# Optimization experiments

Measured on AMD Instinct MI355X. Metric: run time of the kernel, lower is better.

The kernel has to match this reference:

```python
import jax, jax.numpy as jnp
import numpy as np

B, C, L, NLAB, EMB, NFREQ, D = 256, 64, 512, 10, 256, 9, 8
FIN, FH, FOUT = 4 * C, C, C
P_TOTAL = FIN * FH + FH + FH * FOUT + FOUT + FIN * FOUT + FOUT


def _leaky(x):
    return jax.nn.leaky_relu(x, 0.2)


def _conv1d(x, w, b=None, pad=0):
    y = jax.lax.conv_general_dilated(x, w, (1,), [(pad, pad)], dimension_numbers=('NCH', 'OIH', 'NCH'))
    return y if b is None else y + b[None, :, None]


def _res1d(x, w0, b0, w1, b1, ws=None, pad=1):
    # GAN-stability style residual block: out = shortcut(x) + 0.1 * conv1(act(conv0(act(x))))
    xs = _conv1d(x, ws) if ws is not None else x
    dx = _conv1d(_leaky(x), w0, b0, pad)
    dx = _conv1d(_leaky(dx), w1, b1, pad)
    return xs + 0.1 * dx


def _pos_enc():
    # sinusoidal positional encoding, 2*NFREQ channels over L positions
    p = np.arange(L, dtype=np.float32)
    f = (np.pi / 2.0 ** np.arange(NFREQ, dtype=np.float32))[:, None]
    pe = np.concatenate([np.sin(f * p), np.cos(f * p)], axis=0)  # [2*NFREQ, L]
    return jnp.asarray(pe)


def _sobel_kernels():
    s = np.array([1.0, 2.0, 1.0], np.float32)
    d = np.array([-1.0, 0.0, 1.0], np.float32)
    kx = np.einsum('i,j,k->ijk', d, s, s)
    ky = np.einsum('i,j,k->ijk', s, d, s)
    kz = np.einsum('i,j,k->ijk', s, s, d)
    return jnp.asarray(np.stack([kx, ky, kz]))  # [3, 3, 3, 3]


def _sin_sobel(x, k):
    # depthwise 3D sobel along each axis, sin of gradients, concat with input -> 4C channels
    outs = [x]
    for i in range(3):
        w = jnp.broadcast_to(k[i][None, None], (C, 1, 3, 3, 3))
        g = jax.lax.conv_general_dilated(x, w, (1, 1, 1), [(1, 1)] * 3,
                                         dimension_numbers=('NCDHW', 'OIDHW', 'NCDHW'),
                                         feature_group_count=C)
        outs.append(jnp.sin(g))
    return jnp.concatenate(outs, axis=1)


def _inst_norm(x):
    m = x.mean(axis=(2, 3, 4), keepdims=True)
    v = x.var(axis=(2, 3, 4), keepdims=True)
    return (x - m) * jax.lax.rsqrt(v + 1e-5)


def _dyna(x, p):
    # hypernet-generated per-sample 1x1x1 residual conv block
    b = x.shape[0]
    xf = x.reshape(b, FIN, D * D * D)
    o = FIN * FH
    wh = p[:, :o].reshape(b, FH, FIN)
    bh = p[:, o:o + FH]; o += FH
    wl = p[:, o:o + FH * FOUT].reshape(b, FOUT, FH); o += FH * FOUT
    bl = p[:, o:o + FOUT]; o += FOUT
    ws = p[:, o:o + FIN * FOUT].reshape(b, FOUT, FIN); o += FIN * FOUT
    bs = p[:, o:o + FOUT]
    xs = jnp.einsum('boi,bis->bos', ws, xf) + bs[:, :, None]
    dx = _leaky(jnp.einsum('bhi,bis->bhs', wh, xf) + bh[:, :, None])
    dx = jnp.einsum('boh,bhs->bos', wl, dx) + bl[:, :, None]
    return (xs + 0.1 * dx).reshape(b, FOUT, D, D, D)


def _forward(codes, y, fc_w, fc_b, in_w0, in_b0, in_w1, in_b1, in_ws, leak, hyper_w, hyper_b,
             out_w0, out_b0, out_w1, out_b1, l1_w0, l1_b0, l1_w1, l1_b1,
             l2_w0, l2_b0, l2_w1, l2_b1, l2_ws):
    b = codes.shape[0]
    yemb = jax.nn.one_hot(y, NLAB, dtype=codes.dtype) @ fc_w.T + fc_b
    yemb = yemb / jnp.maximum(jnp.linalg.norm(yemb, axis=1, keepdims=True), 1e-12)
    pe = jnp.broadcast_to(_pos_enc()[None], (b, 2 * NFREQ, L))
    x = jnp.concatenate([codes, pe], axis=1)  # [B, C+2*NFREQ, L]
    x = _res1d(x, in_w0, in_b0, in_w1, in_b1, ws=in_ws)
    x = x.reshape(b, C, D, D, D)
    leak_c = jnp.clip(leak, 0.001, 1000.0)
    p = yemb @ hyper_w.T + hyper_b  # per-sample dynamic conv params [B, P_TOTAL]
    k = _sobel_kernels()
    for _ in range(8):
        xn = _inst_norm(x)
        xn = _sin_sobel(xn, k)
        xn = _dyna(xn, p)
        x = x + leak_c * xn
    x = x.reshape(b, C, L)
    x = _res1d(x, out_w0, out_b0, out_w1, out_b1)
    code_idx = jnp.argmax(codes, axis=1).reshape(b * L)
    logits = x.transpose(0, 2, 1).reshape(b * L, C)
    logp = jax.nn.log_softmax(logits, axis=-1)
    loss_cent = -jnp.take_along_axis(logp, code_idx[:, None], axis=1).mean()
    lat = _res1d(x, l1_w0, l1_b0, l1_w1, l1_b1, pad=0)
    lat = _res1d(lat, l2_w0, l2_b0, l2_w1, l2_b1, ws=l2_ws, pad=0)
    return lat[:, 0, :], loss_cent


def setup_inputs() -> dict:
    key = jax.random.key(0)
    ks = jax.random.split(key, 16)
    w = lambda k, s: 0.02 * jax.random.normal(k, s, jnp.float32)
    z = lambda s: jnp.zeros(s, jnp.float32)
    CIN = C + 2 * NFREQ  # 82
    return {
        'codes': jax.random.normal(ks[0], (B, C, L), jnp.float32),
        'y': jax.random.randint(ks[1], (B,), 0, NLAB),
        'fc_w': w(ks[2], (EMB, NLAB)), 'fc_b': z((EMB,)),
        'in_w0': w(ks[3], (C, CIN, 3)), 'in_b0': z((C,)),
        'in_w1': w(ks[4], (C, C, 3)), 'in_b1': z((C,)),
        'in_ws': w(ks[5], (C, CIN, 1)),
        'leak': jnp.asarray(0.1, jnp.float32),
        'hyper_w': w(ks[6], (P_TOTAL, EMB)), 'hyper_b': z((P_TOTAL,)),
        'out_w0': w(ks[7], (C, C, 3)), 'out_b0': z((C,)),
        'out_w1': w(ks[8], (C, C, 3)), 'out_b1': z((C,)),
        'l1_w0': w(ks[9], (C, C, 1)), 'l1_b0': z((C,)),
        'l1_w1': w(ks[10], (C, C, 1)), 'l1_b1': z((C,)),
        'l2_w0': w(ks[11], (1, C, 1)), 'l2_b0': z((1,)),
        'l2_w1': w(ks[12], (1, 1, 1)), 'l2_b1': z((1,)),
        'l2_ws': w(ks[13], (1, C, 1)),
    }


def reference(codes, y, fc_w, fc_b, in_w0, in_b0, in_w1, in_b1, in_ws, leak, hyper_w, hyper_b,
              out_w0, out_b0, out_w1, out_b1, l1_w0, l1_b0, l1_w1, l1_b1,
              l2_w0, l2_b0, l2_w1, l2_b1, l2_ws):
    return _forward(codes, y, fc_w, fc_b, in_w0, in_b0, in_w1, in_b1, in_ws, leak, hyper_w, hyper_b,
                    out_w0, out_b0, out_w1, out_b1, l1_w0, l1_b0, l1_w1, l1_b1,
                    l2_w0, l2_b0, l2_w1, l2_b1, l2_ws)
```

## Files before the change

### kernel.cpp

```cpp
#include <hip/hip_runtime.h>

#define B_ 256
#define C_ 64
#define L_ 512
#define CIN_ 82
#define NFREQ_ 9
#define EMB_ 256
#define NLAB_ 10
#define PT_ 37056
#define OFF_BH 16384
#define OFF_WL 16448
#define OFF_BL 20544
#define OFF_WS 20608
#define OFF_BS 36992
#define PI_F 3.14159265358979323846f

typedef short bh8 __attribute__((ext_vector_type(8)));
typedef float f32x4 __attribute__((ext_vector_type(4)));

__device__ inline float lrelu(float v){ return v > 0.f ? v : 0.2f*v; }

__device__ inline unsigned short f2bf(float f){
  unsigned u = __float_as_uint(f);
  u += 0x7FFFu + ((u >> 16) & 1u);
  return (unsigned short)(u >> 16);
}
__device__ inline float bf2f(unsigned short u){
  return __uint_as_float((unsigned)u << 16);
}
__device__ inline unsigned pk2(float a, float b){
  return (unsigned)f2bf(a) | ((unsigned)f2bf(b) << 16);
}
__device__ inline bh8 cvt8(float4 a, float4 b){
  bh8 r;
  r[0]=(short)f2bf(a.x); r[1]=(short)f2bf(a.y); r[2]=(short)f2bf(a.z); r[3]=(short)f2bf(a.w);
  r[4]=(short)f2bf(b.x); r[5]=(short)f2bf(b.y); r[6]=(short)f2bf(b.z); r[7]=(short)f2bf(b.w);
  return r;
}

__global__ __launch_bounds__(256) void k_yemb(const float* __restrict__ fc_w,
    const float* __restrict__ fc_b, const int* __restrict__ y,
    unsigned short* __restrict__ ybf, float* __restrict__ out){
  int b = blockIdx.x, e = threadIdx.x;
  int lab = y[b];
  float v = fc_w[e*NLAB_ + lab] + fc_b[e];
  __shared__ float red[256];
  red[e] = v*v; __syncthreads();
  for (int s = 128; s; s >>= 1){ if (e < s) red[e] += red[e+s]; __syncthreads(); }
  float nrm = fmaxf(sqrtf(red[0]), 1e-12f);
  ybf[(size_t)b*EMB_ + e] = f2bf(v / nrm);
  if (b == 0 && e == 0) out[B_*L_] = 0.f;
}

__global__ __launch_bounds__(256) void k_hyper(const float* __restrict__ hw,
    const float* __restrict__ hb, const unsigned short* __restrict__ ybf,
    unsigned short* __restrict__ p_bf){
  int tid = threadIdx.x;
  int wid = tid >> 6, lane = tid & 63, col = lane & 15, quad = lane >> 4;
  int j = blockIdx.x*64 + wid*16 + col;
  f32x4 acc[16];
  f32x4 z4 = {0.f,0.f,0.f,0.f};
  #pragma unroll
  for (int i = 0; i < 16; i++) acc[i] = z4;
  for (int k0 = 0; k0 < 256; k0 += 32){
    const float* hp = hw + (size_t)j*EMB_ + k0 + quad*8;
    bh8 bf = cvt8(*(const float4*)hp, *(const float4*)(hp+4));
    #pragma unroll
    for (int mt = 0; mt < 16; mt++){
      bh8 af = *(const bh8*)&ybf[(size_t)(mt*16 + col)*EMB_ + k0 + quad*8];
      acc[mt] = __builtin_amdgcn_mfma_f32_16x16x32_bf16(af, bf, acc[mt], 0, 0, 0);
    }
  }
  float hbv = hb[j];
  #pragma unroll
  for (int mt = 0; mt < 16; mt++){
    int b0 = mt*16 + quad*4;
    #pragma unroll
    for (int r = 0; r < 4; r++)
      p_bf[(size_t)(b0 + r)*PT_ + j] = f2bf(acc[mt][r] + hbv);
  }
}

__device__ inline float pe_raw(int fi, int l){
  if (fi < NFREQ_) return __sinf(PI_F / (float)(1 << fi) * (float)l);
  return __cosf(PI_F / (float)(1 << (fi - NFREQ_)) * (float)l);
}

__global__ __launch_bounds__(256) void k_conv_in1(const float* __restrict__ codes,
    const float* __restrict__ w0, const float* __restrict__ b0,
    unsigned short* __restrict__ t1bf){
  int b = blockIdx.x, l0 = blockIdx.y*128, tid = threadIdx.x;
  int wid = tid>>6, lane = tid&63, col = lane&15, quad = lane>>4;
  __shared__ __attribute__((aligned(16))) unsigned short xT[136][96];
  __shared__ __attribute__((aligned(16))) unsigned short wA[3][64][96];
  for (int i = tid; i < 64*96; i += 256){
    int m = i / 96, cin = i % 96;
    if (cin < CIN_){
      const float* s = w0 + (size_t)m*(CIN_*3) + cin*3;
      wA[0][m][cin] = f2bf(s[0]); wA[1][m][cin] = f2bf(s[1]); wA[2][m][cin] = f2bf(s[2]);
    } else { wA[0][m][cin] = 0; wA[1][m][cin] = 0; wA[2][m][cin] = 0; }
  }
  const float* cb = codes + (size_t)b*C_*L_;
  for (int i = tid; i < 96*34; i += 256){
    int c = i / 34, g = i % 34;
    int lg = l0 - 4 + 4*g;
    #pragma unroll
    for (int r2 = 0; r2 < 4; r2++){
      int l = lg + r2;
      float xv = 0.f;
      if (l >= 0 && l < L_){
        if (c < C_) xv = cb[(size_t)c*L_ + l];
        else if (c < CIN_) xv = pe_raw(c - C_, l);
      }
      xT[4*g + r2][c] = f2bf(lrelu(xv));
    }
  }
  __syncthreads();
  f32x4 z4 = {0.f,0.f,0.f,0.f};
  f32x4 acc[8];
  #pragma unroll
  for (int i = 0; i < 8; i++) acc[i] = z4;
  #pragma unroll
  for (int t = 0; t < 3; t++){
    #pragma unroll
    for (int k0 = 0; k0 < 96; k0 += 32){
      bh8 bfr[2];
      #pragma unroll
      for (int nt = 0; nt < 2; nt++)
        bfr[nt] = *(const bh8*)&xT[wid*32 + nt*16 + col + t + 3][k0 + quad*8];
      #pragma unroll
      for (int mt = 0; mt < 4; mt++){
        bh8 af = *(const bh8*)&wA[t][mt*16 + col][k0 + quad*8];
        #pragma unroll
        for (int nt = 0; nt < 2; nt++)
          acc[mt*2+nt] = __builtin_amdgcn_mfma_f32_16x16x32_bf16(af, bfr[nt], acc[mt*2+nt], 0,0,0);
      }
    }
  }
  #pragma unroll
  for (int mt = 0; mt < 4; mt++){
    int f0 = mt*16 + quad*4;
    float q0 = b0[f0], q1 = b0[f0+1], q2 = b0[f0+2], q3 = b0[f0+3];
    #pragma unroll
    for (int nt = 0; nt < 2; nt++){
      int l = l0 + wid*32 + nt*16 + col;
      f32x4 a = acc[mt*2+nt];
      uint2 o = { pk2(lrelu(a[0]+q0), lrelu(a[1]+q1)),
                  pk2(lrelu(a[2]+q2), lrelu(a[3]+q3)) };
      *(uint2*)&t1bf[((size_t)b*L_ + l)*64 + f0] = o;
    }
  }
}

__global__ __launch_bounds__(256) void k_conv_in2(const float* __restrict__ codes,
    const float* __restrict__ wsp, const float* __restrict__ w1, const float* __restrict__ b1,
    const unsigned short* __restrict__ t1bf, float* __restrict__ x){
  int b = blockIdx.x, l0 = blockIdx.y*128, tid = threadIdx.x;
  int wid = tid>>6, lane = tid&63, col = lane&15, quad = lane>>4;
  __shared__ __attribute__((aligned(16))) unsigned short xT[128][96];
  __shared__ __attribute__((aligned(16))) unsigned short wsA[64][96];
  __shared__ __attribute__((aligned(16))) unsigned short w1A[3][64][72];
  for (int i = tid; i < 64*96; i += 256){
    int m = i / 96, cin = i % 96;
    wsA[m][cin] = (cin < CIN_) ? f2bf(wsp[(size_t)m*CIN_ + cin]) : (unsigned short)0;
  }
  for (int i = tid; i < 64*64; i += 256){
    int m = i >> 6, cin = i & 63;
    const float* s = w1 + (size_t)m*192 + cin*3;
    w1A[0][m][cin] = f2bf(s[0]); w1A[1][m][cin] = f2bf(s[1]); w1A[2][m][cin] = f2bf(s[2]);
  }
  const float* cb = codes + (size_t)b*C_*L_;
  for (int i = tid; i < 96*32; i += 256){
    int c = i / 32, g = i % 32;
    int lg = l0 + 4*g;
    #pragma unroll
    for (int r2 = 0; r2 < 4; r2++){
      int l = lg + r2;
      float xv;
      if (c < C_) xv = cb[(size_t)c*L_ + l];
      else if (c < CIN_) xv = pe_raw(c - C_, l);
      else xv = 0.f;
      xT[4*g + r2][c] = f2bf(xv);
    }
  }
  __syncthreads();
  f32x4 z4 = {0.f,0.f,0.f,0.f};
  f32x4 accS[8], accD[8];
  #pragma unroll
  for (int i = 0; i < 8; i++){ accS[i] = z4; accD[i] = z4; }
  #pragma unroll
  for (int k0 = 0; k0 < 96; k0 += 32){
    bh8 bfr[2];
    #pragma unroll
    for (int nt = 0; nt < 2; nt++)
      bfr[nt] = *(const bh8*)&xT[wid*32 + nt*16 + col][k0 + quad*8];
    #pragma unroll
    for (int mt = 0; mt < 4; mt++){
      bh8 af = *(const bh8*)&wsA[mt*16 + col][k0 + quad*8];
      #pragma unroll
      for (int nt = 0; nt < 2; nt++)
        accS[mt*2+nt] = __builtin_amdgcn_mfma_f32_16x16x32_bf16(af, bfr[nt], accS[mt*2+nt], 0,0,0);
    }
  }
  bh8 zz8 = {0,0,0,0,0,0,0,0};
  #pragma unroll
  for (int t = 0; t < 3; t++){
    #pragma unroll
    for (int k0 = 0; k0 < 64; k0 += 32){
      bh8 bfr[2];
      #pragma unroll
      for (int nt = 0; nt < 2; nt++){
        int l = l0 + wid*32 + nt*16 + col + t - 1;
        bfr[nt] = (l >= 0 && l < L_)
          ? *(const bh8*)&t1bf[((size_t)b*L_ + l)*64 + k0 + quad*8] : zz8;
      }
      #pragma unroll
      for (int mt = 0; mt < 4; mt++){
        bh8 af = *(const bh8*)&w1A[t][mt*16 + col][k0 + quad*8];
        #pragma unroll
        for (int nt = 0; nt < 2; nt++)
          accD[mt*2+nt] = __builtin_amdgcn_mfma_f32_16x16x32_bf16(af, bfr[nt], accD[mt*2+nt], 0,0,0);
      }
    }
  }
  #pragma unroll
  for (int mt = 0; mt < 4; mt++){
    int f0 = mt*16 + quad*4;
    float q0 = b1[f0], q1 = b1[f0+1], q2 = b1[f0+2], q3 = b1[f0+3];
    #pragma unroll
    for (int nt = 0; nt < 2; nt++){
      int l = l0 + wid*32 + nt*16 + col;
      f32x4 s = accS[mt*2+nt], d = accD[mt*2+nt];
      size_t base = ((size_t)b*C_ + f0)*L_ + l;
      x[base]        = s[0] + 0.1f*(d[0] + q0);
      x[base + L_]   = s[1] + 0.1f*(d[1] + q1);
      x[base + 2*L_] = s[2] + 0.1f*(d[2] + q2);
      x[base + 3*L_] = s[3] + 0.1f*(d[3] + q3);
    }
  }
}

__global__ __launch_bounds__(256) void k_feat(const float* __restrict__ x,
    unsigned short* __restrict__ feat){
  int wid = threadIdx.x >> 6, lane = threadIdx.x & 63;
  int gi = blockIdx.x*4 + wid;
  const float* xr = x + (size_t)gi*L_ + lane*8;
  float4 v0 = *(const float4*)xr;
  float4 v1 = *(const float4*)(xr + 4);
  float r[8] = { v0.x, v0.y, v0.z, v0.w, v1.x, v1.y, v1.z, v1.w };
  float s1 = 0.f, s2 = 0.f;
  #pragma unroll
  for (int i = 0; i < 8; i++){ s1 += r[i]; s2 += r[i]*r[i]; }
  for (int m = 32; m; m >>= 1){ s1 += __shfl_xor(s1, m); s2 += __shfl_xor(s2, m); }
  float mean = s1 * (1.f/512.f);
  float rstd = rsqrtf(s2*(1.f/512.f) - mean*mean + 1e-5f);
  float xn[8];
  #pragma unroll
  for (int i = 0; i < 8; i++) xn[i] = (r[i] - mean) * rstd;

  size_t fb = ((size_t)(gi >> 6)*4*C_ + (gi & 63))*L_ + lane*8;
  { uint4 o = { pk2(xn[0],xn[1]), pk2(xn[2],xn[3]), pk2(xn[4],xn[5]), pk2(xn[6],xn[7]) };
    *(uint4*)(feat + fb) = o; }

  __shared__ float S[4][5][64][8];
  float A[8], Bv[8];
  A[0] = 2.f*xn[0] + xn[1];           Bv[0] = xn[1];
  #pragma unroll
  for (int i = 1; i < 7; i++){ A[i] = xn[i-1] + 2.f*xn[i] + xn[i+1]; Bv[i] = xn[i+1] - xn[i-1]; }
  A[7] = xn[6] + 2.f*xn[7];           Bv[7] = -xn[6];
  { float4 a0 = {A[0],A[1],A[2],A[3]}, a1 = {A[4],A[5],A[6],A[7]};
    float4 b0 = {Bv[0],Bv[1],Bv[2],Bv[3]}, b1 = {Bv[4],Bv[5],Bv[6],Bv[7]};
    *(float4*)&S[wid][0][lane][0] = a0; *(float4*)&S[wid][0][lane][4] = a1;
    *(float4*)&S[wid][1][lane][0] = b0; *(float4*)&S[wid][1][lane][4] = b1; }
  __syncthreads();

  int yy = lane & 7, zz = lane >> 3;
  int lm = (yy > 0) ? lane-1 : lane;  float wm = (yy > 0) ? 1.f : 0.f;
  int lp = (yy < 7) ? lane+1 : lane;  float wp = (yy < 7) ? 1.f : 0.f;
  float Am[8], Ap[8], Bm[8], Bp[8];
  { float4 u0, u1;
    u0 = *(const float4*)&S[wid][0][lm][0]; u1 = *(const float4*)&S[wid][0][lm][4];
    Am[0]=u0.x*wm; Am[1]=u0.y*wm; Am[2]=u0.z*wm; Am[3]=u0.w*wm; Am[4]=u1.x*wm; Am[5]=u1.y*wm; Am[6]=u1.z*wm; Am[7]=u1.w*wm;
    u0 = *(const float4*)&S[wid][0][lp][0]; u1 = *(const float4*)&S[wid][0][lp][4];
    Ap[0]=u0.x*wp; Ap[1]=u0.y*wp; Ap[2]=u0.z*wp; Ap[3]=u0.w*wp; Ap[4]=u1.x*wp; Ap[5]=u1.y*wp; Ap[6]=u1.z*wp; Ap[7]=u1.w*wp;
    u0 = *(const float4*)&S[wid][1][lm][0]; u1 = *(const float4*)&S[wid][1][lm][4];
    Bm[0]=u0.x*wm; Bm[1]=u0.y*wm; Bm[2]=u0.z*wm; Bm[3]=u0.w*wm; Bm[4]=u1.x*wm; Bm[5]=u1.y*wm; Bm[6]=u1.z*wm; Bm[7]=u1.w*wm;
    u0 = *(const float4*)&S[wid][1][lp][0]; u1 = *(const float4*)&S[wid][1][lp][4];
    Bp[0]=u0.x*wp; Bp[1]=u0.y*wp; Bp[2]=u0.z*wp; Bp[3]=u0.w*wp; Bp[4]=u1.x*wp; Bp[5]=u1.y*wp; Bp[6]=u1.z*wp; Bp[7]=u1.w*wp;
  }
  float Cv[8], Dv[8], Ev[8];
  #pragma unroll
  for (int i = 0; i < 8; i++){
    Cv[i] = Am[i] + 2.f*A[i] + Ap[i];
    Dv[i] = Ap[i] - Am[i];
    Ev[i] = Bm[i] + 2.f*Bv[i] + Bp[i];
  }
  { float4 c0={Cv[0],Cv[1],Cv[2],Cv[3]}, c1={Cv[4],Cv[5],Cv[6],Cv[7]};
    float4 d0={Dv[0],Dv[1],Dv[2],Dv[3]}, d1={Dv[4],Dv[5],Dv[6],Dv[7]};
    float4 e0={Ev[0],Ev[1],Ev[2],Ev[3]}, e1={Ev[4],Ev[5],Ev[6],Ev[7]};
    *(float4*)&S[wid][2][lane][0]=c0; *(float4*)&S[wid][2][lane][4]=c1;
    *(float4*)&S[wid][3][lane][0]=d0; *(float4*)&S[wid][3][lane][4]=d1;
    *(float4*)&S[wid][4][lane][0]=e0; *(float4*)&S[wid][4][lane][4]=e1; }
  __syncthreads();

  int zm = (zz > 0) ? lane-8 : lane;  float qm = (zz > 0) ? 1.f : 0.f;
  int zp = (zz < 7) ? lane+8 : lane;  float qp = (zz < 7) ? 1.f : 0.f;
  float g0[8], g1[8], g2[8];
  { float4 u0, u1, w0, w1;
    u0 = *(const float4*)&S[wid][2][zm][0]; u1 = *(const float4*)&S[wid][2][zm][4];
    w0 = *(const float4*)&S[wid][2][zp][0]; w1 = *(const float4*)&S[wid][2][zp][4];
    g0[0]=w0.x*qp-u0.x*qm; g0[1]=w0.y*qp-u0.y*qm; g0[2]=w0.z*qp-u0.z*qm; g0[3]=w0.w*qp-u0.w*qm;
    g0[4]=w1.x*qp-u1.x*qm; g0[5]=w1.y*qp-u1.y*qm; g0[6]=w1.z*qp-u1.z*qm; g0[7]=w1.w*qp-u1.w*qm;
    u0 = *(const float4*)&S[wid][3][zm][0]; u1 = *(const float4*)&S[wid][3][zm][4];
    w0 = *(const float4*)&S[wid][3][zp][0]; w1 = *(const float4*)&S[wid][3][zp][4];
    g1[0]=u0.x*qm+2.f*Dv[0]+w0.x*qp; g1[1]=u0.y*qm+2.f*Dv[1]+w0.y*qp;
    g1[2]=u0.z*qm+2.f*Dv[2]+w0.z*qp; g1[3]=u0.w*qm+2.f*Dv[3]+w0.w*qp;
    g1[4]=u1.x*qm+2.f*Dv[4]+w1.x*qp; g1[5]=u1.y*qm+2.f*Dv[5]+w1.y*qp;
    g1[6]=u1.z*qm+2.f*Dv[6]+w1.z*qp; g1[7]=u1.w*qm+2.f*Dv[7]+w1.w*qp;
    u0 = *(const float4*)&S[wid][4][zm][0]; u1 = *(const float4*)&S[wid][4][zm][4];
    w0 = *(const float4*)&S[wid][4][zp][0]; w1 = *(const float4*)&S[wid][4][zp][4];
    g2[0]=u0.x*qm+2.f*Ev[0]+w0.x*qp; g2[1]=u0.y*qm+2.f*Ev[1]+w0.y*qp;
    g2[2]=u0.z*qm+2.f*Ev[2]+w0.z*qp; g2[3]=u0.w*qm+2.f*Ev[3]+w0.w*qp;
    g2[4]=u1.x*qm+2.f*Ev[4]+w1.x*qp; g2[5]=u1.y*qm+2.f*Ev[5]+w1.y*qp;
    g2[6]=u1.z*qm+2.f*Ev[6]+w1.z*qp; g2[7]=u1.w*qm+2.f*Ev[7]+w1.w*qp;
  }
  { uint4 o = { pk2(__sinf(g0[0]),__sinf(g0[1])), pk2(__sinf(g0[2]),__sinf(g0[3])),
                pk2(__sinf(g0[4]),__sinf(g0[5])), pk2(__sinf(g0[6]),__sinf(g0[7])) };
    *(uint4*)(feat + fb + (size_t)C_*L_) = o; }
  { uint4 o = { pk2(__sinf(g1[0]),__sinf(g1[1])), pk2(__sinf(g1[2]),__sinf(g1[3])),
                pk2(__sinf(g1[4]),__sinf(g1[5])), pk2(__sinf(g1[6]),__sinf(g1[7])) };
    *(uint4*)(feat + fb + (size_t)2*C_*L_) = o; }
  { uint4 o = { pk2(__sinf(g2[0]),__sinf(g2[1])), pk2(__sinf(g2[2]),__sinf(g2[3])),
                pk2(__sinf(g2[4]),__sinf(g2[5])), pk2(__sinf(g2[6]),__sinf(g2[7])) };
    *(uint4*)(feat + fb + (size_t)3*C_*L_) = o; }
}

__global__ __launch_bounds__(256) void k_dyna(float* __restrict__ x,
    const unsigned short* __restrict__ feat, const unsigned short* __restrict__ p_bf,
    const float* __restrict__ leak){
  int b = blockIdx.x, tid = threadIdx.x;
  int wid = tid >> 6, lane = tid & 63, col = lane & 15, quad = lane >> 4;
  int s0 = blockIdx.y * 256;
  int ncol = s0 + wid*64;
  const unsigned short* pb = p_bf + (size_t)b*PT_;
  const unsigned short* fbase = feat + (size_t)b*4*C_*L_;
  __shared__ __attribute__((aligned(16))) unsigned short h_t[256][72];

  f32x4 zz4 = {0.f, 0.f, 0.f, 0.f};
  f32x4 acc_h[16], acc_s[16];
  #pragma unroll
  for (int i = 0; i < 16; i++){ acc_h[i] = zz4; acc_s[i] = zz4; }

  for (int k0 = 0; k0 < 256; k0 += 32){
    bh8 bf[4];
    #pragma unroll
    for (int nt = 0; nt < 4; nt++){
      const unsigned short* src = fbase + (size_t)(k0 + quad*8)*L_ + ncol + nt*16 + col;
      bh8 t;
      #pragma unroll
      for (int j = 0; j < 8; j++) t[j] = (short)src[(size_t)j*L_];
      bf[nt] = t;
    }
    #pragma unroll
    for (int mt = 0; mt < 4; mt++){
      int m = mt*16 + col;
      bh8 ah = *(const bh8*)&pb[(size_t)m*256 + k0 + quad*8];
      bh8 aw = *(const bh8*)&pb[OFF_WS + (size_t)m*256 + k0 + quad*8];
      #pragma unroll
      for (int nt = 0; nt < 4; nt++){
        acc_h[mt*4+nt] = __builtin_amdgcn_mfma_f32_16x16x32_bf16(ah, bf[nt], acc_h[mt*4+nt], 0, 0, 0);
        acc_s[mt*4+nt] = __builtin_amdgcn_mfma_f32_16x16x32_bf16(aw, bf[nt], acc_s[mt*4+nt], 0, 0, 0);
      }
    }
  }
  #pragma unroll
  for (int mt = 0; mt < 4; mt++){
    int f0 = mt*16 + quad*4;
    float bh0 = bf2f(pb[OFF_BH+f0]), bh1 = bf2f(pb[OFF_BH+f0+1]);
    float bh2 = bf2f(pb[OFF_BH+f0+2]), bh3 = bf2f(pb[OFF_BH+f0+3]);
    #pragma unroll
    for (int nt = 0; nt < 4; nt++){
      int n = wid*64 + nt*16 + col;
      f32x4 a = acc_h[mt*4+nt];
      uint2 o = { pk2(lrelu(a[0]+bh0), lrelu(a[1]+bh1)),
                  pk2(lrelu(a[2]+bh2), lrelu(a[3]+bh3)) };
      *(uint2*)&h_t[n][f0] = o;
    }
  }
  __syncthreads();
  f32x4 acc2[16];
  #pragma unroll
  for (int i = 0; i < 16; i++) acc2[i] = zz4;
  #pragma unroll
  for (int k0 = 0; k0 < 64; k0 += 32){
    bh8 hb[4];
    #pragma unroll
    for (int nt = 0; nt < 4; nt++){
      int n = wid*64 + nt*16 + col;
      hb[nt] = *(const bh8*)&h_t[n][k0 + quad*8];
    }
    #pragma unroll
    for (int mt = 0; mt < 4; mt++){
      bh8 al = *(const bh8*)&pb[OFF_WL + (size_t)(mt*16 + col)*64 + k0 + quad*8];
      #pragma unroll
      for (int nt = 0; nt < 4; nt++)
        acc2[mt*4+nt] = __builtin_amdgcn_mfma_f32_16x16x32_bf16(al, hb[nt], acc2[mt*4+nt], 0, 0, 0);
    }
  }
  float lk = fminf(fmaxf(leak[0], 0.001f), 1000.f);
  #pragma unroll
  for (int mt = 0; mt < 4; mt++){
    int f0 = mt*16 + quad*4;
    float bs0 = bf2f(pb[OFF_BS+f0]), bs1 = bf2f(pb[OFF_BS+f0+1]);
    float bs2 = bf2f(pb[OFF_BS+f0+2]), bs3 = bf2f(pb[OFF_BS+f0+3]);
    float bl0 = bf2f(pb[OFF_BL+f0]), bl1 = bf2f(pb[OFF_BL+f0+1]);
    float bl2 = bf2f(pb[OFF_BL+f0+2]), bl3 = bf2f(pb[OFF_BL+f0+3]);
    #pragma unroll
    for (int nt = 0; nt < 4; nt++){
      int s = ncol + nt*16 + col;
      f32x4 xs = acc_s[mt*4+nt], dx = acc2[mt*4+nt];
      float ov0 = xs[0] + bs0 + 0.1f*(dx[0] + bl0);
      float ov1 = xs[1] + bs1 + 0.1f*(dx[1] + bl1);
      float ov2 = xs[2] + bs2 + 0.1f*(dx[2] + bl2);
      float ov3 = xs[3] + bs3 + 0.1f*(dx[3] + bl3);
      size_t xi = ((size_t)b*C_ + f0)*L_ + s;
      x[xi]          += lk*ov0;
      x[xi + L_]     += lk*ov1;
      x[xi + 2*L_]   += lk*ov2;
      x[xi + 3*L_]   += lk*ov3;
    }
  }
}

__global__ __launch_bounds__(256) void k_conv_out1(const float* __restrict__ x,
    const float* __restrict__ w, const float* __restrict__ bias,
    unsigned short* __restrict__ t1bf){
  int b = blockIdx.x, l0 = blockIdx.y*128, tid = threadIdx.x;
  int wid = tid>>6, lane = tid&63, col = lane&15, quad = lane>>4;
  __shared__ __attribute__((aligned(16))) unsigned short xT[136][72];
  __shared__ __attribute__((aligned(16))) unsigned short wA[3][64][72];
  for (int i = tid; i < 64*64; i += 256){
    int m = i >> 6, cin = i & 63;
    const float* s = w + (size_t)m*192 + cin*3;
    wA[0][m][cin] = f2bf(s[0]); wA[1][m][cin] = f2bf(s[1]); wA[2][m][cin] = f2bf(s[2]);
  }
  const float* xb = x + (size_t)b*C_*L_;
  for (int i = tid; i < 64*34; i += 256){
    int c = i / 34, g = i % 34;
    int lg = l0 - 4 + 4*g;
    if (lg >= 0 && lg + 3 < L_){
      float4 f = *(const float4*)&xb[(size_t)c*L_ + lg];
      xT[4*g  ][c] = f2bf(lrelu(f.x));
      xT[4*g+1][c] = f2bf(lrelu(f.y));
      xT[4*g+2][c] = f2bf(lrelu(f.z));
      xT[4*g+3][c] = f2bf(lrelu(f.w));
    } else {
      #pragma unroll
      for (int r2 = 0; r2 < 4; r2++){
        int l = lg + r2;
        float v = (l >= 0 && l < L_) ? xb[(size_t)c*L_ + l] : 0.f;
        xT[4*g + r2][c] = f2bf(lrelu(v));
      }
    }
  }
  __syncthreads();
  f32x4 z4 = {0.f,0.f,0.f,0.f};
  f32x4 acc[8];
  #pragma unroll
  for (int i = 0; i < 8; i++) acc[i] = z4;
  #pragma unroll
  for (int t = 0; t < 3; t++){
    #pragma unroll
    for (int k0 = 0; k0 < 64; k0 += 32){
      bh8 bfr[2];
      #pragma unroll
      for (int nt = 0; nt < 2; nt++)
        bfr[nt] = *(const bh8*)&xT[wid*32 + nt*16 + col + t + 3][k0 + quad*8];
      #pragma unroll
      for (int mt = 0; mt < 4; mt++){
        bh8 af = *(const bh8*)&wA[t][mt*16 + col][k0 + quad*8];
        #pragma unroll
        for (int nt = 0; nt < 2; nt++)
          acc[mt*2+nt] = __builtin_amdgcn_mfma_f32_16x16x32_bf16(af, bfr[nt], acc[mt*2+nt], 0,0,0);
      }
    }
  }
  #pragma unroll
  for (int mt = 0; mt < 4; mt++){
    int f0 = mt*16 + quad*4;
    float q0 = bias[f0], q1 = bias[f0+1], q2 = bias[f0+2], q3 = bias[f0+3];
    #pragma unroll
    for (int nt = 0; nt < 2; nt++){
// ... 155 lines not shown
    bh8 bfr[4];
    #pragma unroll
    for (int nt = 0; nt < 4; nt++)
      bfr[nt] = *(const bh8*)&Bt[wid*64 + nt*16 + col][k0 + quad*8];
    #pragma unroll
    for (int mt = 0; mt < 4; mt++){
      bh8 af = *(const bh8*)&wA[1][mt*16 + col][k0 + quad*8];
      #pragma unroll
      for (int nt = 0; nt < 4; nt++)
        acc2[mt*4+nt] = __builtin_amdgcn_mfma_f32_16x16x32_bf16(af, bfr[nt], acc2[mt*4+nt], 0, 0, 0);
    }
  }
  float psA[4] = {0.f,0.f,0.f,0.f}, psB[4] = {0.f,0.f,0.f,0.f};
  #pragma unroll
  for (int mt = 0; mt < 4; mt++){
    int f0 = mt*16 + quad*4;
    f32x4 b11v = *(const f32x4*)&b11[f0];
    f32x4 wsv  = *(const f32x4*)&ws2[f0];
    f32x4 w20v = *(const f32x4*)&w20[f0];
    #pragma unroll
    for (int nt = 0; nt < 4; nt++){
      int lg = l0 + wid*64 + nt*16 + col;
      size_t base = ((size_t)b*C_ + f0)*L_ + lg;
      f32x4 a = acc2[mt*4+nt];
      #pragma unroll
      for (int r = 0; r < 4; r++){
        float xv = x[base + (size_t)r*L_];
        float lat = xv + 0.1f*(a[r] + b11v[r]);
        psA[nt] += wsv[r]*lat;
        psB[nt] += w20v[r]*lrelu(lat);
      }
    }
  }
  #pragma unroll
  for (int nt = 0; nt < 4; nt++){
    psA[nt] += __shfl_xor(psA[nt], 16); psA[nt] += __shfl_xor(psA[nt], 32);
    psB[nt] += __shfl_xor(psB[nt], 16); psB[nt] += __shfl_xor(psB[nt], 32);
  }
  if (quad == 0){
    float b20s = b20[0], w21s = w21[0], b21s = b21[0];
    #pragma unroll
    for (int nt = 0; nt < 4; nt++){
      float dx2 = w21s*lrelu(psB[nt] + b20s) + b21s;
      out[(size_t)b*L_ + l0 + wid*64 + nt*16 + col] = psA[nt] + 0.1f*dx2;
    }
  }
}

extern "C" void kernel_launch(void* const* d_in, const int* in_sizes, int n_in,
                              void* d_out, int out_size, void* d_ws, size_t ws_size,
                              hipStream_t stream) {
  (void)in_sizes; (void)n_in; (void)out_size; (void)ws_size;
  const float* codes   = (const float*)d_in[0];
  const int*   y       = (const int*)  d_in[1];
  const float* fc_w    = (const float*)d_in[2];
  const float* fc_b    = (const float*)d_in[3];
  const float* in_w0   = (const float*)d_in[4];
  const float* in_b0   = (const float*)d_in[5];
  const float* in_w1   = (const float*)d_in[6];
  const float* in_b1   = (const float*)d_in[7];
  const float* in_wsp  = (const float*)d_in[8];
  const float* leak    = (const float*)d_in[9];
  const float* hyper_w = (const float*)d_in[10];
  const float* hyper_b = (const float*)d_in[11];
  const float* out_w0  = (const float*)d_in[12];
  const float* out_b0  = (const float*)d_in[13];
  const float* out_w1  = (const float*)d_in[14];
  const float* out_b1  = (const float*)d_in[15];
  const float* l1_w0   = (const float*)d_in[16];
  const float* l1_b0   = (const float*)d_in[17];
  const float* l1_w1   = (const float*)d_in[18];
  const float* l1_b1   = (const float*)d_in[19];
  const float* l2_w0   = (const float*)d_in[20];
  const float* l2_b0   = (const float*)d_in[21];
  const float* l2_w1   = (const float*)d_in[22];
  const float* l2_b1   = (const float*)d_in[23];
  const float* l2_ws   = (const float*)d_in[24];
  float* out = (float*)d_out;

  char* ws = (char*)d_ws;
  unsigned short* p_bf = (unsigned short*)(ws);
  unsigned short* ybf  = (unsigned short*)(ws + 18972672);
  float* x             = (float*)(ws + 19103744);
  unsigned short* feat = (unsigned short*)(ws + 52658176);
  unsigned short* t1bf = (unsigned short*)(ws + 52658176);

  k_yemb<<<B_, 256, 0, stream>>>(fc_w, fc_b, y, ybf, out);
  k_hyper<<<PT_/64, 256, 0, stream>>>(hyper_w, hyper_b, ybf, p_bf);
  k_conv_in1<<<dim3(B_, 4), 256, 0, stream>>>(codes, in_w0, in_b0, t1bf);
  k_conv_in2<<<dim3(B_, 4), 256, 0, stream>>>(codes, in_wsp, in_w1, in_b1, t1bf, x);
  for (int it = 0; it < 8; ++it){
    k_feat<<<B_*C_/4, 256, 0, stream>>>(x, feat);
    k_dyna<<<dim3(B_, 2), 256, 0, stream>>>(x, feat, p_bf, leak);
  }
  k_conv_out1<<<dim3(B_, 4), 256, 0, stream>>>(x, out_w0, out_b0, t1bf);
  k_conv_out2<<<dim3(B_, 2), 256, 0, stream>>>(x, t1bf, out_w1, out_b1);
  k_loss<<<dim3(B_, 2), 256, 0, stream>>>(x, codes, out);
  k_lat<<<dim3(B_, 2), 256, 0, stream>>>(x, l1_w0, l1_b0, l1_w1, l1_b1,
                                         l2_w0, l2_b0, l2_w1, l2_b1, l2_ws, out);
}
```

Before: 916.1 us.

## Fuse instance-norm/sobel feature build into dynamic conv kernel, drop feat buffer

Merges the per-iteration feature kernel (instance norm, separable 3D Sobel, sin) into the hypernet dynamic-conv kernel. Features are now built chunk by chunk in shared memory with wave shuffles instead of round-tripping a 4C x L bf16 tensor through global memory. The hypernet output columns are permuted so each chunk's interleaved channel order matches the weight layout. It also pads LDS arrays in the input convs to reduce bank conflicts. The cost is that each of the two blocks per sample recomputes the full-sample stats and features, discarding the half it does not own.

Measured after the change: 1.064 ms. +16.2%, slower.

```diff
diff --git a/kernel.cpp b/kernel.cpp
--- a/kernel.cpp
+++ b/kernel.cpp
@@ -37,6 +37,20 @@
   r[4]=(short)f2bf(b.x); r[5]=(short)f2bf(b.y); r[6]=(short)f2bf(b.z); r[7]=(short)f2bf(b.w);
   return r;
 }
+__device__ inline bh8 ld8(const unsigned short* p){
+  union { uint2 u[2]; bh8 v; } t;
+  t.u[0] = *(const uint2*)p; t.u[1] = *(const uint2*)(p+4);
+  return t.v;
+}
+
+__device__ inline int perm_j(int j){
+  if (j < OFF_BH){ int m = j >> 8, i = j & 255; return (m << 8) + ((i & 63) << 2) + (i >> 6); }
+  if (j >= OFF_WS && j < OFF_BS){
+    int jj = j - OFF_WS; int m = jj >> 8, i = jj & 255;
+    return OFF_WS + (m << 8) + ((i & 63) << 2) + (i >> 6);
+  }
+  return j;
+}
 
 __global__ __launch_bounds__(256) void k_yemb(const float* __restrict__ fc_w,
     const float* __restrict__ fc_b, const int* __restrict__ y,
@@ -72,12 +86,13 @@
     }
   }
   float hbv = hb[j];
+  int jd = perm_j(j);
   #pragma unroll
   for (int mt = 0; mt < 16; mt++){
     int b0 = mt*16 + quad*4;
     #pragma unroll
     for (int r = 0; r < 4; r++)
-      p_bf[(size_t)(b0 + r)*PT_ + j] = f2bf(acc[mt][r] + hbv);
+      p_bf[(size_t)(b0 + r)*PT_ + jd] = f2bf(acc[mt][r] + hbv);
   }
 }
 
@@ -91,28 +106,25 @@
     unsigned short* __restrict__ t1bf){
   int b = blockIdx.x, l0 = blockIdx.y*128, tid = threadIdx.x;
   int wid = tid>>6, lane = tid&63, col = lane&15, quad = lane>>4;
-  __shared__ __attribute__((aligned(16))) unsigned short xT[136][96];
-  __shared__ __attribute__((aligned(16))) unsigned short wA[3][64][96];
-  for (int i = tid; i < 64*96; i += 256){
-    int m = i / 96, cin = i % 96;
-    if (cin < CIN_){
-      const float* s = w0 + (size_t)m*(CIN_*3) + cin*3;
-      wA[0][m][cin] = f2bf(s[0]); wA[1][m][cin] = f2bf(s[1]); wA[2][m][cin] = f2bf(s[2]);
-    } else { wA[0][m][cin] = 0; wA[1][m][cin] = 0; wA[2][m][cin] = 0; }
+  __shared__ __attribute__((aligned(16))) unsigned short xT[132][104];
+  __shared__ __attribute__((aligned(16))) unsigned short wAi[64][296];
+  for (int i = tid; i < 64*288; i += 256){
+    int m = i / 288, rem = i % 288, t = rem / 96, cin = rem % 96;
+    wAi[m][t*96 + cin] = (cin < CIN_) ? f2bf(w0[(size_t)m*(CIN_*3) + cin*3 + t]) : (unsigned short)0;
   }
   const float* cb = codes + (size_t)b*C_*L_;
-  for (int i = tid; i < 96*34; i += 256){
-    int c = i / 34, g = i % 34;
-    int lg = l0 - 4 + 4*g;
+  for (int i = tid; i < 96*33; i += 256){
+    int c = i / 33, g = i % 33;
     #pragma unroll
     for (int r2 = 0; r2 < 4; r2++){
-      int l = lg + r2;
+      int row = 4*g + r2;
+      int l = l0 - 1 + row;
       float xv = 0.f;
       if (l >= 0 && l < L_){
         if (c < C_) xv = cb[(size_t)c*L_ + l];
         else if (c < CIN_) xv = pe_raw(c - C_, l);
       }
-      xT[4*g + r2][c] = f2bf(lrelu(xv));
+      xT[row][c] = f2bf(lrelu(xv));
     }
   }
   __syncthreads();
@@ -127,10 +139,10 @@
       bh8 bfr[2];
       #pragma unroll
       for (int nt = 0; nt < 2; nt++)
-        bfr[nt] = *(const bh8*)&xT[wid*32 + nt*16 + col + t + 3][k0 + quad*8];
+        bfr[nt] = *(const bh8*)&xT[wid*32 + nt*16 + col + t][k0 + quad*8];
       #pragma unroll
       for (int mt = 0; mt < 4; mt++){
-        bh8 af = *(const bh8*)&wA[t][mt*16 + col][k0 + quad*8];
+        bh8 af = *(const bh8*)&wAi[mt*16 + col][t*96 + k0 + quad*8];
         #pragma unroll
         for (int nt = 0; nt < 2; nt++)
           acc[mt*2+nt] = __builtin_amdgcn_mfma_f32_16x16x32_bf16(af, bfr[nt], acc[mt*2+nt], 0,0,0);
@@ -157,9 +169,9 @@
     const unsigned short* __restrict__ t1bf, float* __restrict__ x){
   int b = blockIdx.x, l0 = blockIdx.y*128, tid = threadIdx.x;
   int wid = tid>>6, lane = tid&63, col = lane&15, quad = lane>>4;
-  __shared__ __attribute__((aligned(16))) unsigned short xT[128][96];
-  __shared__ __attribute__((aligned(16))) unsigned short wsA[64][96];
-  __shared__ __attribute__((aligned(16))) unsigned short w1A[3][64][72];
+  __shared__ __attribute__((aligned(16))) unsigned short xT[128][100];
+  __shared__ __attribute__((aligned(16))) unsigned short wsA[64][100];
+  __shared__ __attribute__((aligned(16))) unsigned short w1A[3][64][68];
   for (int i = tid; i < 64*96; i += 256){
     int m = i / 96, cin = i % 96;
     wsA[m][cin] = (cin < CIN_) ? f2bf(wsp[(size_t)m*CIN_ + cin]) : (unsigned short)0;
@@ -193,10 +205,10 @@
     bh8 bfr[2];
     #pragma unroll
     for (int nt = 0; nt < 2; nt++)
-      bfr[nt] = *(const bh8*)&xT[wid*32 + nt*16 + col][k0 + quad*8];
+      bfr[nt] = ld8(&xT[wid*32 + nt*16 + col][k0 + quad*8]);
     #pragma unroll
     for (int mt = 0; mt < 4; mt++){
-      bh8 af = *(const bh8*)&wsA[mt*16 + col][k0 + quad*8];
+      bh8 af = ld8(&wsA[mt*16 + col][k0 + quad*8]);
       #pragma unroll
       for (int nt = 0; nt < 2; nt++)
         accS[mt*2+nt] = __builtin_amdgcn_mfma_f32_16x16x32_bf16(af, bfr[nt], accS[mt*2+nt], 0,0,0);
@@ -216,7 +228,7 @@
       }
       #pragma unroll
       for (int mt = 0; mt < 4; mt++){
-        bh8 af = *(const bh8*)&w1A[t][mt*16 + col][k0 + quad*8];
+        bh8 af = ld8(&w1A[t][mt*16 + col][k0 + quad*8]);
         #pragma unroll
         for (int nt = 0; nt < 2; nt++)
           accD[mt*2+nt] = __builtin_amdgcn_mfma_f32_16x16x32_bf16(af, bfr[nt], accD[mt*2+nt], 0,0,0);
@@ -240,139 +252,111 @@
   }
 }
 
-__global__ __launch_bounds__(256) void k_feat(const float* __restrict__ x,
-    unsigned short* __restrict__ feat){
-  int wid = threadIdx.x >> 6, lane = threadIdx.x & 63;
-  int gi = blockIdx.x*4 + wid;
-  const float* xr = x + (size_t)gi*L_ + lane*8;
-  float4 v0 = *(const float4*)xr;
-  float4 v1 = *(const float4*)(xr + 4);
-  float r[8] = { v0.x, v0.y, v0.z, v0.w, v1.x, v1.y, v1.z, v1.w };
-  float s1 = 0.f, s2 = 0.f;
-  #pragma unroll
-  for (int i = 0; i < 8; i++){ s1 += r[i]; s2 += r[i]*r[i]; }
-  for (int m = 32; m; m >>= 1){ s1 += __shfl_xor(s1, m); s2 += __shfl_xor(s2, m); }
-  float mean = s1 * (1.f/512.f);
-  float rstd = rsqrtf(s2*(1.f/512.f) - mean*mean + 1e-5f);
-  float xn[8];
-  #pragma unroll
-  for (int i = 0; i < 8; i++) xn[i] = (r[i] - mean) * rstd;
-
-  size_t fb = ((size_t)(gi >> 6)*4*C_ + (gi & 63))*L_ + lane*8;
-  { uint4 o = { pk2(xn[0],xn[1]), pk2(xn[2],xn[3]), pk2(xn[4],xn[5]), pk2(xn[6],xn[7]) };
-    *(uint4*)(feat + fb) = o; }
-
-  __shared__ float S[4][5][64][8];
-  float A[8], Bv[8];
-  A[0] = 2.f*xn[0] + xn[1];           Bv[0] = xn[1];
-  #pragma unroll
-  for (int i = 1; i < 7; i++){ A[i] = xn[i-1] + 2.f*xn[i] + xn[i+1]; Bv[i] = xn[i+1] - xn[i-1]; }
-  A[7] = xn[6] + 2.f*xn[7];           Bv[7] = -xn[6];
-  { float4 a0 = {A[0],A[1],A[2],A[3]}, a1 = {A[4],A[5],A[6],A[7]};
-    float4 b0 = {Bv[0],Bv[1],Bv[2],Bv[3]}, b1 = {Bv[4],Bv[5],Bv[6],Bv[7]};
-    *(float4*)&S[wid][0][lane][0] = a0; *(float4*)&S[wid][0][lane][4] = a1;
-    *(float4*)&S[wid][1][lane][0] = b0; *(float4*)&S[wid][1][lane][4] = b1; }
+__global__ __launch_bounds__(256, 2) void k_iter(float* __restrict__ x,
+    const unsigned short* __restrict__ p_bf, const float* __restrict__ leak){
+  int b = blockIdx.x, yblk = blockIdx.y, tid = threadIdx.x;
+  int wid = tid >> 6, lane = tid & 63, col = lane & 15, quad = lane >> 4;
+  int l0 = yblk * 256;
+  const unsigned short* pb = p_bf + (size_t)b*PT_;
+  const float* xb = x + (size_t)b*C_*L_;
+
+  __shared__ __attribute__((aligned(16))) unsigned short fch[256][40];
+  __shared__ __attribute__((aligned(16))) unsigned short h_t[256][72];
+  __shared__ float sm[64], sr[64];
+
+  for (int t = 0; t < 16; t++){
+    int c = t*4 + wid;
+    const float* xr = xb + (size_t)c*L_ + lane*8;
+    float4 v0 = *(const float4*)xr, v1 = *(const float4*)(xr+4);
+    float s1 = v0.x+v0.y+v0.z+v0.w + v1.x+v1.y+v1.z+v1.w;
+    float s2 = v0.x*v0.x+v0.y*v0.y+v0.z*v0.z+v0.w*v0.w
+             + v1.x*v1.x+v1.y*v1.y+v1.z*v1.z+v1.w*v1.w;
+    #pragma unroll
+    for (int m = 32; m; m >>= 1){ s1 += __shfl_xor(s1, m); s2 += __shfl_xor(s2, m); }
+    if (lane == 0){
+      float mean = s1 * (1.f/512.f);
+      sm[c] = mean;
+      sr[c] = rsqrtf(s2*(1.f/512.f) - mean*mean + 1e-5f);
+    }
+  }
   __syncthreads();
 
-  int yy = lane & 7, zz = lane >> 3;
-  int lm = (yy > 0) ? lane-1 : lane;  float wm = (yy > 0) ? 1.f : 0.f;
-  int lp = (yy < 7) ? lane+1 : lane;  float wp = (yy < 7) ? 1.f : 0.f;
-  float Am[8], Ap[8], Bm[8], Bp[8];
-  { float4 u0, u1;
-    u0 = *(const float4*)&S[wid][0][lm][0]; u1 = *(const float4*)&S[wid][0][lm][4];
-    Am[0]=u0.x*wm; Am[1]=u0.y*wm; Am[2]=u0.z*wm; Am[3]=u0.w*wm; Am[4]=u1.x*wm; Am[5]=u1.y*wm; Am[6]=u1.z*wm; Am[7]=u1.w*wm;
-    u0 = *(const float4*)&S[wid][0][lp][0]; u1 = *(const float4*)&S[wid][0][lp][4];
-    Ap[0]=u0.x*wp; Ap[1]=u0.y*wp; Ap[2]=u0.z*wp; Ap[3]=u0.w*wp; Ap[4]=u1.x*wp; Ap[5]=u1.y*wp; Ap[6]=u1.z*wp; Ap[7]=u1.w*wp;
-    u0 = *(const float4*)&S[wid][1][lm][0]; u1 = *(const float4*)&S[wid][1][lm][4];
-    Bm[0]=u0.x*wm; Bm[1]=u0.y*wm; Bm[2]=u0.z*wm; Bm[3]=u0.w*wm; Bm[4]=u1.x*wm; Bm[5]=u1.y*wm; Bm[6]=u1.z*wm; Bm[7]=u1.w*wm;
-    u0 = *(const float4*)&S[wid][1][lp][0]; u1 = *(const float4*)&S[wid][1][lp][4];
-    Bp[0]=u0.x*wp; Bp[1]=u0.y*wp; Bp[2]=u0.z*wp; Bp[3]=u0.w*wp; Bp[4]=u1.x*wp; Bp[5]=u1.y*wp; Bp[6]=u1.z*wp; Bp[7]=u1.w*wp;
-  }
-  float Cv[8], Dv[8], Ev[8];
-  #pragma unroll
-  for (int i = 0; i < 8; i++){
-    Cv[i] = Am[i] + 2.f*A[i] + Ap[i];
-    Dv[i] = Ap[i] - Am[i];
-    Ev[i] = Bm[i] + 2.f*Bv[i] + Bp[i];
-  }
-  { float4 c0={Cv[0],Cv[1],Cv[2],Cv[3]}, c1={Cv[4],Cv[5],Cv[6],Cv[7]};
-    float4 d0={Dv[0],Dv[1],Dv[2],Dv[3]}, d1={Dv[4],Dv[5],Dv[6],Dv[7]};
-    float4 e0={Ev[0],Ev[1],Ev[2],Ev[3]}, e1={Ev[4],Ev[5],Ev[6],Ev[7]};
-    *(float4*)&S[wid][2][lane][0]=c0; *(float4*)&S[wid][2][lane][4]=c1;
-    *(float4*)&S[wid][3][lane][0]=d0; *(float4*)&S[wid][3][lane][4]=d1;
-    *(float4*)&S[wid][4][lane][0]=e0; *(float4*)&S[wid][4][lane][4]=e1; }
-  __syncthreads();
-
-  int zm = (zz > 0) ? lane-8 : lane;  float qm = (zz > 0) ? 1.f : 0.f;
-  int zp = (zz < 7) ? lane+8 : lane;  float qp = (zz < 7) ? 1.f : 0.f;
-  float g0[8], g1[8], g2[8];
-  { float4 u0, u1, w0, w1;
-    u0 = *(const float4*)&S[wid][2][zm][0]; u1 = *(const float4*)&S[wid][2][zm][4];
-    w0 = *(const float4*)&S[wid][2][zp][0]; w1 = *(const float4*)&S[wid][2][zp][4];
-    g0[0]=w0.x*qp-u0.x*qm; g0[1]=w0.y*qp-u0.y*qm; g0[2]=w0.z*qp-u0.z*qm; g0[3]=w0.w*qp-u0.w*qm;
-    g0[4]=w1.x*qp-u1.x*qm; g0[5]=w1.y*qp-u1.y*qm; g0[6]=w1.z*qp-u1.z*qm; g0[7]=w1.w*qp-u1.w*qm;
-    u0 = *(const float4*)&S[wid][3][zm][0]; u1 = *(const float4*)&S[wid][3][zm][4];
-    w0 = *(const float4*)&S[wid][3][zp][0]; w1 = *(const float4*)&S[wid][3][zp][4];
-    g1[0]=u0.x*qm+2.f*Dv[0]+w0.x*qp; g1[1]=u0.y*qm+2.f*Dv[1]+w0.y*qp;
-    g1[2]=u0.z*qm+2.f*Dv[2]+w0.z*qp; g1[3]=u0.w*qm+2.f*Dv[3]+w0.w*qp;
-    g1[4]=u1.x*qm+2.f*Dv[4]+w1.x*qp; g1[5]=u1.y*qm+2.f*Dv[5]+w1.y*qp;
-    g1[6]=u1.z*qm+2.f*Dv[6]+w1.z*qp; g1[7]=u1.w*qm+2.f*Dv[7]+w1.w*qp;
-    u0 = *(const float4*)&S[wid][4][zm][0]; u1 = *(const float4*)&S[wid][4][zm][4];
-    w0 = *(const float4*)&S[wid][4][zp][0]; w1 = *(const float4*)&S[wid][4][zp][4];
-    g2[0]=u0.x*qm+2.f*Ev[0]+w0.x*qp; g2[1]=u0.y*qm+2.f*Ev[1]+w0.y*qp;
-    g2[2]=u0.z*qm+2.f*Ev[2]+w0.z*qp; g2[3]=u0.w*qm+2.f*Ev[3]+w0.w*qp;
-    g2[4]=u1.x*qm+2.f*Ev[4]+w1.x*qp; g2[5]=u1.y*qm+2.f*Ev[5]+w1.y*qp;
-    g2[6]=u1.z*qm+2.f*Ev[6]+w1.z*qp; g2[7]=u1.w*qm+2.f*Ev[7]+w1.w*qp;
-  }
-  { uint4 o = { pk2(__sinf(g0[0]),__sinf(g0[1])), pk2(__sinf(g0[2]),__sinf(g0[3])),
-                pk2(__sinf(g0[4]),__sinf(g0[5])), pk2(__sinf(g0[6]),__sinf(g0[7])) };
-    *(uint4*)(feat + fb + (size_t)C_*L_) = o; }
-  { uint4 o = { pk2(__sinf(g1[0]),__sinf(g1[1])), pk2(__sinf(g1[2]),__sinf(g1[3])),
-                pk2(__sinf(g1[4]),__sinf(g1[5])), pk2(__sinf(g1[6]),__sinf(g1[7])) };
-    *(uint4*)(feat + fb + (size_t)2*C_*L_) = o; }
-  { uint4 o = { pk2(__sinf(g2[0]),__sinf(g2[1])), pk2(__sinf(g2[2]),__sinf(g2[3])),
-                pk2(__sinf(g2[4]),__sinf(g2[5])), pk2(__sinf(g2[6]),__sinf(g2[7])) };
-    *(uint4*)(feat + fb + (size_t)3*C_*L_) = o; }
-}
-
-__global__ __launch_bounds__(256) void k_dyna(float* __restrict__ x,
-    const unsigned short* __restrict__ feat, const unsigned short* __restrict__ p_bf,
-    const float* __restrict__ leak){
-  int b = blockIdx.x, tid = threadIdx.x;
-  int wid = tid >> 6, lane = tid & 63, col = lane & 15, quad = lane >> 4;
-  int s0 = blockIdx.y * 256;
-  int ncol = s0 + wid*64;
-  const unsigned short* pb = p_bf + (size_t)b*PT_;
-  const unsigned short* fbase = feat + (size_t)b*4*C_*L_;
-  __shared__ __attribute__((aligned(16))) unsigned short h_t[256][72];
-
-  f32x4 zz4 = {0.f, 0.f, 0.f, 0.f};
+  f32x4 zz4 = {0.f,0.f,0.f,0.f};
   f32x4 acc_h[16], acc_s[16];
   #pragma unroll
   for (int i = 0; i < 16; i++){ acc_h[i] = zz4; acc_s[i] = zz4; }
 
-  for (int k0 = 0; k0 < 256; k0 += 32){
-    bh8 bf[4];
-    #pragma unroll
-    for (int nt = 0; nt < 4; nt++){
-      const unsigned short* src = fbase + (size_t)(k0 + quad*8)*L_ + ncol + nt*16 + col;
-      bh8 t;
-      #pragma unroll
-      for (int j = 0; j < 8; j++) t[j] = (short)src[(size_t)j*L_];
-      bf[nt] = t;
-    }
+  int yy = lane & 7, zzd = lane >> 3;
+  float wm = (yy > 0) ? 1.f : 0.f, wp = (yy < 7) ? 1.f : 0.f;
+  float qm = (zzd > 0) ? 1.f : 0.f, qp = (zzd < 7) ? 1.f : 0.f;
+  bool active = ((lane >> 5) == yblk);
+
+  for (int ch = 0; ch < 8; ch++){
+    #pragma unroll
+    for (int rr = 0; rr < 2; rr++){
+      int cc = rr*4 + wid;
+      int c = ch*8 + cc;
+      const float* xr = xb + (size_t)c*L_ + lane*8;
+      float4 v0 = *(const float4*)xr, v1 = *(const float4*)(xr+4);
+      float r8[8] = { v0.x, v0.y, v0.z, v0.w, v1.x, v1.y, v1.z, v1.w };
+      float mean = sm[c], rstd = sr[c];
+      float xn[8];
+      #pragma unroll
+      for (int i = 0; i < 8; i++) xn[i] = (r8[i] - mean) * rstd;
+      float A[8], Bv[8];
+      A[0] = 2.f*xn[0] + xn[1];  Bv[0] = xn[1];
+      #pragma unroll
+      for (int i = 1; i < 7; i++){ A[i] = xn[i-1] + 2.f*xn[i] + xn[i+1]; Bv[i] = xn[i+1] - xn[i-1]; }
+      A[7] = xn[6] + 2.f*xn[7];  Bv[7] = -xn[6];
+      float Cv[8], Dv[8], Ev[8];
+      #pragma unroll
+      for (int i = 0; i < 8; i++){
+        float am = __shfl_up(A[i], 1)*wm,  ap = __shfl_down(A[i], 1)*wp;
+        float bm = __shfl_up(Bv[i], 1)*wm, bp = __shfl_down(Bv[i], 1)*wp;
+        Cv[i] = am + 2.f*A[i] + ap;
+        Dv[i] = ap - am;
+        Ev[i] = bm + 2.f*Bv[i] + bp;
+      }
+      uint2 val[8];
+      #pragma unroll
+      for (int i = 0; i < 8; i++){
+        float cm = __shfl_up(Cv[i], 8)*qm, cp = __shfl_down(Cv[i], 8)*qp;
+        float dm = __shfl_up(Dv[i], 8)*qm, dp = __shfl_down(Dv[i], 8)*qp;
+        float em = __shfl_up(Ev[i], 8)*qm, ep = __shfl_down(Ev[i], 8)*qp;
+        float G0 = cp - cm;
+        float G1 = dm + 2.f*Dv[i] + dp;
+        float G2 = em + 2.f*Ev[i] + ep;
+        val[i].x = pk2(xn[i], __sinf(G0));
+        val[i].y = pk2(__sinf(G1), __sinf(G2));
+      }
+      if (active){
+        int lrow = (lane & 31) * 8;
+        #pragma unroll
+        for (int j = 0; j < 8; j++){
+          int i = (j + yy) & 7;
+          *(uint2*)&fch[lrow + i][cc*4] = val[i];
+        }
+      }
+    }
+    __syncthreads();
+    bh8 bfr[4];
+    #pragma unroll
+    for (int nt = 0; nt < 4; nt++)
+      bfr[nt] = *(const bh8*)&fch[wid*64 + nt*16 + col][quad*8];
     #pragma unroll
     for (int mt = 0; mt < 4; mt++){
       int m = mt*16 + col;
-      bh8 ah = *(const bh8*)&pb[(size_t)m*256 + k0 + quad*8];
-      bh8 aw = *(const bh8*)&pb[OFF_WS + (size_t)m*256 + k0 + quad*8];
+      bh8 ah = *(const bh8*)&pb[(size_t)m*256 + ch*32 + quad*8];
+      bh8 aw = *(const bh8*)&pb[OFF_WS + (size_t)m*256 + ch*32 + quad*8];
       #pragma unroll
       for (int nt = 0; nt < 4; nt++){
-        acc_h[mt*4+nt] = __builtin_amdgcn_mfma_f32_16x16x32_bf16(ah, bf[nt], acc_h[mt*4+nt], 0, 0, 0);
-        acc_s[mt*4+nt] = __builtin_amdgcn_mfma_f32_16x16x32_bf16(aw, bf[nt], acc_s[mt*4+nt], 0, 0, 0);
-      }
-    }
-  }
+        acc_h[mt*4+nt] = __builtin_amdgcn_mfma_f32_16x16x32_bf16(ah, bfr[nt], acc_h[mt*4+nt], 0, 0, 0);
+        acc_s[mt*4+nt] = __builtin_amdgcn_mfma_f32_16x16x32_bf16(aw, bfr[nt], acc_s[mt*4+nt], 0, 0, 0);
+      }
+    }
+    __syncthreads();
+  }
+
   #pragma unroll
   for (int mt = 0; mt < 4; mt++){
     int f0 = mt*16 + quad*4;
@@ -395,10 +379,8 @@
   for (int k0 = 0; k0 < 64; k0 += 32){
     bh8 hb[4];
     #pragma unroll
-    for (int nt = 0; nt < 4; nt++){
-      int n = wid*64 + nt*16 + col;
-      hb[nt] = *(const bh8*)&h_t[n][k0 + quad*8];
-    }
+    for (int nt = 0; nt < 4; nt++)
+      hb[nt] = *(const bh8*)&h_t[wid*64 + nt*16 + col][k0 + quad*8];
     #pragma unroll
     for (int mt = 0; mt < 4; mt++){
       bh8 al = *(const bh8*)&pb[OFF_WL + (size_t)(mt*16 + col)*64 + k0 + quad*8];
@@ -408,6 +390,7 @@
     }
   }
   float lk = fminf(fmaxf(leak[0], 0.001f), 1000.f);
+  int ncol = l0 + wid*64;
   #pragma unroll
   for (int mt = 0; mt < 4; mt++){
     int f0 = mt*16 + quad*4;
@@ -729,7 +712,6 @@
   unsigned short* p_bf = (unsigned short*)(ws);
   unsigned short* ybf  = (unsigned short*)(ws + 18972672);
   float* x             = (float*)(ws + 19103744);
-  unsigned short* feat = (unsigned short*)(ws + 52658176);
   unsigned short* t1bf = (unsigned short*)(ws + 52658176);
 
   k_yemb<<<B_, 256, 0, stream>>>(fc_w, fc_b, y, ybf, out);
@@ -737,8 +719,7 @@
   k_conv_in1<<<dim3(B_, 4), 256, 0, stream>>>(codes, in_w0, in_b0, t1bf);
   k_conv_in2<<<dim3(B_, 4), 256, 0, stream>>>(codes, in_wsp, in_w1, in_b1, t1bf, x);
   for (int it = 0; it < 8; ++it){
-    k_feat<<<B_*C_/4, 256, 0, stream>>>(x, feat);
-    k_dyna<<<dim3(B_, 2), 256, 0, stream>>>(x, feat, p_bf, leak);
+    k_iter<<<dim3(B_, 2), 256, 0, stream>>>(x, p_bf, leak);
   }
   k_conv_out1<<<dim3(B_, 4), 256, 0, stream>>>(x, out_w0, out_b0, t1bf);
   k_conv_out2<<<dim3(B_, 2), 256, 0, stream>>>(x, t1bf, out_w1, out_b1);
```
